# Kernel tuning notes

Hardware: AMD Instinct MI355X
Metric: run time of the kernel (lower is better)

Reference implementation:

```python
import jax, jax.numpy as jnp
import numpy as np

DIM = 1024
HEADS = 16

def setup_inputs() -> dict:
    key = jax.random.key(0)
    k1, k2, k3, k4 = jax.random.split(key, 4)
    x = jax.random.normal(k1, (2, 2048, DIM), dtype=jnp.float32)
    ln_gamma = jnp.ones((DIM,), dtype=jnp.float32)
    ln_beta = jnp.zeros((DIM,), dtype=jnp.float32)
    # torch Linear weight is [out, in]; store transposed [in, out] for x @ W
    W_qkv = jax.random.normal(k2, (DIM, 3 * DIM), dtype=jnp.float32) * (DIM ** -0.5)
    W_out = jax.random.normal(k3, (DIM, DIM), dtype=jnp.float32) * (DIM ** -0.5)
    b_out = jax.random.normal(k4, (DIM,), dtype=jnp.float32) * 0.02
    return {"x": x, "ln_gamma": ln_gamma, "ln_beta": ln_beta,
            "W_qkv": W_qkv, "W_out": W_out, "b_out": b_out}

def reference(x, ln_gamma, ln_beta, W_qkv, W_out, b_out):
    B, N, C = x.shape
    H = HEADS
    Dh = C // H
    scale = Dh ** -0.5
    # LayerNorm (eps=1e-5, torch default)
    mu = jnp.mean(x, axis=-1, keepdims=True)
    var = jnp.var(x, axis=-1, keepdims=True)
    xn = (x - mu) / jnp.sqrt(var + 1e-5) * ln_gamma + ln_beta
    # QKV projection: [B,N,3C] -> [3,B,H,N,Dh]
    qkv = (xn @ W_qkv).reshape(B, N, 3, H, Dh).transpose(2, 0, 3, 1, 4)
    q, k, v = qkv[0], qkv[1], qkv[2]
    attn = jnp.einsum('bhnd,bhmd->bhnm', q, k) * scale  # [B,H,N,N]
    attn = jax.nn.softmax(attn, axis=-1)
    out = jnp.einsum('bhnm,bhmd->bhnd', attn, v)  # [B,H,N,Dh]
    out = out.transpose(0, 2, 1, 3).reshape(B, N, C)
    return out @ W_out + b_out
```

## Files before the change

kernel.cpp:

```cpp
#include <hip/hip_runtime.h>
#include <hip/hip_bf16.h>

#define DIM 1024
#define HEADS 16
#define DH 64
#define SEQ 2048
#define BATCH 2
#define ROWS (BATCH*SEQ)
#define C3 (3*DIM)
#define NT (SEQ/64)

typedef __attribute__((ext_vector_type(8))) short s16x8;
typedef __attribute__((ext_vector_type(4))) short s16x4;
typedef __attribute__((ext_vector_type(4))) float f32x4;
typedef __attribute__((ext_vector_type(16))) float f32x16;
typedef __attribute__((ext_vector_type(4))) unsigned int u32x4;
typedef __attribute__((ext_vector_type(2))) unsigned int u32x2;

__device__ __forceinline__ void gll16(const void* g, void* l) {
  __builtin_amdgcn_global_load_lds((const __attribute__((address_space(1))) void*)g,
                                   (__attribute__((address_space(3))) void*)l, 16, 0, 0);
}
__device__ __forceinline__ float bf2f(short s) {
  return __builtin_bit_cast(float, ((unsigned)(unsigned short)s) << 16);
}
__device__ __forceinline__ short f2bf(float f) {
  return (short)__bfloat16_as_ushort(__float2bfloat16(f));
}
__device__ __forceinline__ unsigned pk2(float a, float b) {
  unsigned lo = (unsigned)__bfloat16_as_ushort(__float2bfloat16(a));
  unsigned hh = (unsigned)__bfloat16_as_ushort(__float2bfloat16(b));
  return lo | (hh << 16);
}
__device__ __forceinline__ float fexp2(float x) {
#if __has_builtin(__builtin_amdgcn_exp2f)
  return __builtin_amdgcn_exp2f(x);
#else
  float r; asm("v_exp_f32 %0, %1" : "=v"(r) : "v"(x)); return r;
#endif
}

__global__ __launch_bounds__(256) void prep_kernel(const float* __restrict__ x,
    const float* __restrict__ gamma, const float* __restrict__ beta,
    __hip_bfloat16* __restrict__ xn,
    const float* __restrict__ Wqkv, __hip_bfloat16* __restrict__ wqkv_t,
    const float* __restrict__ Wout, __hip_bfloat16* __restrict__ wout_t) {
  const int bid = blockIdx.x;
  const int t = threadIdx.x;
  if (bid < ROWS) {
    __shared__ float red[8];
    const float4* xp = (const float4*)(x + (size_t)bid * DIM);
    float4 v = xp[t];
    float s = v.x + v.y + v.z + v.w;
    float q = v.x*v.x + v.y*v.y + v.z*v.z + v.w*v.w;
    for (int off = 32; off >= 1; off >>= 1) {
      s += __shfl_xor(s, off, 64);
      q += __shfl_xor(q, off, 64);
    }
    int w = t >> 6;
    if ((t & 63) == 0) { red[w] = s; red[4 + w] = q; }
    __syncthreads();
    s = red[0] + red[1] + red[2] + red[3];
    q = red[4] + red[5] + red[6] + red[7];
    float mu = s * (1.0f / DIM);
    float var = q * (1.0f / DIM) - mu * mu;
    float rstd = rsqrtf(var + 1e-5f);
    float4 g4 = ((const float4*)gamma)[t];
    float4 b4 = ((const float4*)beta)[t];
    __hip_bfloat16* op = xn + (size_t)bid * DIM + t * 4;
    op[0] = __float2bfloat16((v.x - mu) * rstd * g4.x + b4.x);
    op[1] = __float2bfloat16((v.y - mu) * rstd * g4.y + b4.y);
    op[2] = __float2bfloat16((v.z - mu) * rstd * g4.z + b4.z);
    op[3] = __float2bfloat16((v.w - mu) * rstd * g4.w + b4.w);
  } else {
    __shared__ float tile[32][33];
    const float* in; __hip_bfloat16* out; int R, Cn, c0, r0;
    if (bid < ROWS + 3072) {
      int id = bid - ROWS;
      in = Wqkv; out = wqkv_t; R = DIM; Cn = C3;
      c0 = (id % 96) * 32; r0 = (id / 96) * 32;
    } else {
      int id = bid - ROWS - 3072;
      in = Wout; out = wout_t; R = DIM; Cn = DIM;
      c0 = (id % 32) * 32; r0 = (id / 32) * 32;
    }
    int tx = t & 31, ty = t >> 5;
#pragma unroll
    for (int i = 0; i < 4; i++)
      tile[ty + i * 8][tx] = in[(size_t)(r0 + ty + i * 8) * Cn + c0 + tx];
    __syncthreads();
#pragma unroll
    for (int i = 0; i < 4; i++)
      out[(size_t)(c0 + ty + i * 8) * R + r0 + tx] = __float2bfloat16(tile[tx][ty + i * 8]);
  }
}

__global__ __launch_bounds__(512) void gemm192(const __hip_bfloat16* __restrict__ A,
    const __hip_bfloat16* __restrict__ Bt, __hip_bfloat16* __restrict__ C,
    int M, int Nc, int K) {
  __shared__ short lds_a[2][256 * 64];
  __shared__ short lds_b[2][192 * 64];
  const int t = threadIdx.x, l = t & 63;
  const int w = t >> 6, wr = w >> 2, wc = w & 3;
  const int m0 = blockIdx.y * 256, n0 = blockIdx.x * 192;
  const short* Ab = (const short*)A;
  const short* Bb = (const short*)Bt;
  f32x4 acc[8][3] = {};
  const int srow = t >> 3;
  const int schk = (t & 7) ^ (srow & 7);
  const int NIT = K / 64;

  {
    char* la = (char*)&lds_a[0][0];
    char* lb = (char*)&lds_b[0][0];
#pragma unroll
    for (int p = 0; p < 4; p++)
      gll16(Ab + (size_t)(m0 + p * 64 + srow) * K + schk * 8, la + p * 8192 + t * 16);
#pragma unroll
    for (int p = 0; p < 3; p++)
      gll16(Bb + (size_t)(n0 + p * 64 + srow) * K + schk * 8, lb + p * 8192 + t * 16);
  }
  for (int it = 0; it < NIT; ++it) {
    const int cur = it & 1;
    __syncthreads();
    if (it + 1 < NIT) {
      const int kk = (it + 1) * 64;
      char* la = (char*)&lds_a[cur ^ 1][0];
      char* lb = (char*)&lds_b[cur ^ 1][0];
#pragma unroll
      for (int p = 0; p < 4; p++)
        gll16(Ab + (size_t)(m0 + p * 64 + srow) * K + kk + schk * 8, la + p * 8192 + t * 16);
#pragma unroll
      for (int p = 0; p < 3; p++)
        gll16(Bb + (size_t)(n0 + p * 64 + srow) * K + kk + schk * 8, lb + p * 8192 + t * 16);
      asm volatile("s_waitcnt vmcnt(7)" ::: "memory");
    } else {
      asm volatile("s_waitcnt vmcnt(0)" ::: "memory");
    }
    __syncthreads();
    const char* la = (const char*)&lds_a[cur][0];
    const char* lb = (const char*)&lds_b[cur][0];
    s16x8 af[4], bf[3];
#define GPH_READ_A(FH, S)                                                     \
    _Pragma("unroll")                                                         \
    for (int f = 0; f < 4; f++) {                                             \
      int row = wr * 128 + (FH * 4 + f) * 16 + (l & 15);                      \
      int chk = (((S) * 4 + (l >> 4)) ^ (l & 7)) * 16;                        \
      af[f] = *(const s16x8*)(la + row * 128 + chk);                          \
    }
#define GPH_READ_B(S)                                                         \
    _Pragma("unroll")                                                         \
    for (int n = 0; n < 3; n++) {                                             \
      int row = wc * 48 + n * 16 + (l & 15);                                  \
      int chk = (((S) * 4 + (l >> 4)) ^ (l & 7)) * 16;                        \
      bf[n] = *(const s16x8*)(lb + row * 128 + chk);                          \
    }
#define GPH_MFMA(FH)                                                          \
    __builtin_amdgcn_s_barrier();                                             \
    asm volatile("s_waitcnt lgkmcnt(0)" ::: "memory");                        \
    __builtin_amdgcn_sched_barrier(0);                                        \
    __builtin_amdgcn_s_setprio(1);                                            \
    _Pragma("unroll")                                                         \
    for (int f = 0; f < 4; f++)                                               \
      _Pragma("unroll")                                                       \
      for (int n = 0; n < 3; n++)                                             \
        acc[FH * 4 + f][n] =                                                  \
            __builtin_amdgcn_mfma_f32_16x16x32_bf16(af[f], bf[n],             \
                                                    acc[FH * 4 + f][n], 0, 0, 0); \
    __builtin_amdgcn_s_setprio(0);                                            \
    __builtin_amdgcn_s_barrier();

    GPH_READ_A(0, 0) GPH_READ_B(0) GPH_MFMA(0)
    GPH_READ_A(1, 0) GPH_MFMA(1)
    GPH_READ_A(0, 1) GPH_READ_B(1) GPH_MFMA(0)
    GPH_READ_A(1, 1) GPH_MFMA(1)
#undef GPH_READ_A
#undef GPH_READ_B
#undef GPH_MFMA
  }
#pragma unroll
  for (int f = 0; f < 8; f++)
#pragma unroll
    for (int n = 0; n < 3; n++) {
      int col = n0 + wc * 48 + n * 16 + (l & 15);
#pragma unroll
      for (int r = 0; r < 4; r++) {
        int row = m0 + wr * 128 + f * 16 + (l >> 4) * 4 + r;
        C[(size_t)row * Nc + col] = __float2bfloat16(acc[f][n][r]);
      }
    }
}

__global__ __launch_bounds__(256) void gemm_out(const __hip_bfloat16* __restrict__ A,
    const __hip_bfloat16* __restrict__ Bt, float* __restrict__ C,
    const float* __restrict__ bias) {
  __shared__ short lds_a[2][128 * 32];
  __shared__ short lds_b[2][64 * 32];
  const int t = threadIdx.x, l = t & 63, w = t >> 6;
  const int wr = w >> 1, wc = w & 1;
  const int m0 = blockIdx.y * 128, n0 = blockIdx.x * 64;
  const short* Ab = (const short*)A;
  const short* Bb = (const short*)Bt;
  const int K = DIM;
  f32x4 acc[4][2] = {};
  const int srow = t >> 2, scol = (t & 3) * 8;
  {
    char* la = (char*)&lds_a[0][0];
    char* lb = (char*)&lds_b[0][0];
    gll16(Ab + (size_t)(m0 + srow) * K + scol,      la + t * 16);
    gll16(Ab + (size_t)(m0 + 64 + srow) * K + scol, la + 4096 + t * 16);
    gll16(Bb + (size_t)(n0 + srow) * K + scol,      lb + t * 16);
  }
  for (int it = 0; it < K / 32; ++it) {
    const int cur = it & 1;
    __syncthreads();
    if (it + 1 < K / 32) {
      const int kk = (it + 1) * 32;
      char* la = (char*)&lds_a[cur ^ 1][0];
      char* lb = (char*)&lds_b[cur ^ 1][0];
      gll16(Ab + (size_t)(m0 + srow) * K + kk + scol,      la + t * 16);
      gll16(Ab + (size_t)(m0 + 64 + srow) * K + kk + scol, la + 4096 + t * 16);
      gll16(Bb + (size_t)(n0 + srow) * K + kk + scol,      lb + t * 16);
      asm volatile("s_waitcnt vmcnt(3)" ::: "memory");
    } else {
      asm volatile("s_waitcnt vmcnt(0)" ::: "memory");
    }
    __syncthreads();
    s16x8 af[4], bf[2];
#pragma unroll
    for (int m = 0; m < 4; m++)
      af[m] = *(const s16x8*)&lds_a[cur][(wr * 64 + m * 16 + (l & 15)) * 32 + (l >> 4) * 8];
#pragma unroll
    for (int n = 0; n < 2; n++)
      bf[n] = *(const s16x8*)&lds_b[cur][(wc * 32 + n * 16 + (l & 15)) * 32 + (l >> 4) * 8];
#pragma unroll
    for (int m = 0; m < 4; m++)
#pragma unroll
      for (int n = 0; n < 2; n++)
        acc[m][n] = __builtin_amdgcn_mfma_f32_16x16x32_bf16(af[m], bf[n], acc[m][n], 0, 0, 0);
  }
#pragma unroll
  for (int m = 0; m < 4; m++)
#pragma unroll
    for (int n = 0; n < 2; n++) {
      int col = n0 + wc * 32 + n * 16 + (l & 15);
      float bb = bias[col];
#pragma unroll
      for (int r = 0; r < 4; r++) {
        int row = m0 + wr * 64 + m * 16 + (l >> 4) * 4 + r;
        C[(size_t)row * DIM + col] = acc[m][n][r] + bb;
      }
    }
}

__global__ __launch_bounds__(512) void attn_kernel(const __hip_bfloat16* __restrict__ qkv,
    __hip_bfloat16* __restrict__ attno) {
  const int t = threadIdx.x, l = t & 63, w = t >> 6;
  const int hi = l >> 5, lq = l & 31;
  const int bid = blockIdx.x;
  const int xcd = bid & 7, j = bid >> 3;
  const int bh = xcd + 8 * (j & 3);
  const int qb = j >> 2;
  const int b = bh >> 4, h = bh & 15;
  const short* base  = (const short*)qkv + (size_t)b * SEQ * C3 + h * DH;
  const short* kbase = base + DIM;
  const short* vbase = base + 2 * DIM;
  const int qr0 = qb * 256 + w * 32;

  __shared__ short kbuf[2][2][64 * 64];
  __shared__ short vbuf[2][2][64 * 64];

  const float SCL = 0.125f * 1.44269504089f;
  s16x8 qf[4];
#pragma unroll
  for (int dk = 0; dk < 4; dk++) {
    s16x8 raw = *(const s16x8*)(base + (size_t)(qr0 + lq) * C3 + dk * 16 + hi * 8);
#pragma unroll
    for (int j2 = 0; j2 < 8; j2++) qf[dk][j2] = f2bf(bf2f(raw[j2]) * SCL);
  }

  s16x8 ones;
#pragma unroll
  for (int j2 = 0; j2 < 8; j2++) ones[j2] = (short)0x3F80;

  f32x16 o0, o1, osum, zf;
#pragma unroll
  for (int r = 0; r < 16; r++) { o0[r] = 0.f; o1[r] = 0.f; osum[r] = 0.f; zf[r] = 0.f; }
  asm volatile("" : "+v"(zf));

  const int krow = t >> 3;
  const int ksrc = (t & 7) ^ (krow & 7);
  const int vr = t & 31, vcg = t >> 5;

#define K_STAGE(DST, ROW0)                                                      \
  gll16(kbase + (size_t)((ROW0) + krow) * C3 + ksrc * 8, (char*)(DST) + t * 16);

#define V_LOAD(VA, VB, ROW0)                                                    \
  VA = __builtin_bit_cast(u32x2, *(const s16x4*)(vbase + (size_t)((ROW0) + 2 * vr) * C3 + vcg * 4)); \
  VB = __builtin_bit_cast(u32x2, *(const s16x4*)(vbase + (size_t)((ROW0) + 2 * vr + 1) * C3 + vcg * 4));

#define V_WRITE(VD, VA, VB)                                                     \
  { char* vd_ = (char*)(VD);                                                    \
    _Pragma("unroll")                                                           \
    for (int i = 0; i < 4; i++) {                                               \
      int d = vcg * 4 + i;                                                      \
      unsigned dw = __builtin_amdgcn_perm((VB)[i >> 1], (VA)[i >> 1],           \
                                          (i & 1) ? 0x07060302u : 0x05040100u); \
      *(unsigned*)(vd_ + d * 128 + (((vr >> 2) ^ (d & 7)) * 16) + (vr & 3) * 4) = dw; } }

  {
    K_STAGE(&kbuf[0][0][0], 0)
    K_STAGE(&kbuf[0][1][0], 64)
    u32x2 va0, vb0, va1, vb1;
    V_LOAD(va0, vb0, 0)
    V_LOAD(va1, vb1, 64)
    V_WRITE(&vbuf[0][0][0], va0, vb0)
    V_WRITE(&vbuf[0][1][0], va1, vb1)
  }
  __syncthreads();

#define QK_SUB(KB, S0, S1)                                                      \
  {                                                                             \
    const char* kb_ = (const char*)(KB);                                        \
    { int chk0 = (hi ^ (l & 7)) * 16;                                           \
      s16x8 kf0 = *(const s16x8*)(kb_ + (size_t)lq * 128 + chk0);               \
      s16x8 kf1 = *(const s16x8*)(kb_ + (size_t)(32 + lq) * 128 + chk0);        \
      S0 = __builtin_amdgcn_mfma_f32_32x32x16_bf16(kf0, qf[0], zf, 0, 0, 0);    \
      S1 = __builtin_amdgcn_mfma_f32_32x32x16_bf16(kf1, qf[0], zf, 0, 0, 0); }  \
    _Pragma("unroll")                                                           \
    for (int dk = 1; dk < 4; dk++) {                                            \
      int chk = ((2 * dk + hi) ^ (l & 7)) * 16;                                 \
      s16x8 kf0 = *(const s16x8*)(kb_ + (size_t)lq * 128 + chk);                \
      s16x8 kf1 = *(const s16x8*)(kb_ + (size_t)(32 + lq) * 128 + chk);         \
      S0 = __builtin_amdgcn_mfma_f32_32x32x16_bf16(kf0, qf[dk], S0, 0, 0, 0);   \
      S1 = __builtin_amdgcn_mfma_f32_32x32x16_bf16(kf1, qf[dk], S1, 0, 0, 0);   \
    }                                                                           \
  }

#define SMPV_SUB(S0, S1, VB)                                                    \
  {                                                                             \
    const char* vbp_ = (const char*)(VB);                                       \
    _Pragma("unroll")                                                           \
    for (int r = 0; r < 16; r++) { S0[r] = fexp2(S0[r]); S1[r] = fexp2(S1[r]); }\
    _Pragma("unroll")                                                           \
    for (int n = 0; n < 2; n++) {                                               \
      const f32x16& stn = n ? S1 : S0;                                          \
      _Pragma("unroll")                                                         \
      for (int ksl = 0; ksl < 2; ksl++) {                                       \
        int rb = ksl * 8;                                                       \
        int a_ = (int)pk2(stn[rb + 0], stn[rb + 1]);                            \
        int b_ = (int)pk2(stn[rb + 2], stn[rb + 3]);                            \
        int c_ = (int)pk2(stn[rb + 4], stn[rb + 5]);                            \
        int d_ = (int)pk2(stn[rb + 6], stn[rb + 7]);                            \
        asm volatile("v_permlane32_swap_b32 %0, %1" : "+v"(a_), "+v"(c_));      \
        asm volatile("v_permlane32_swap_b32 %0, %1" : "+v"(b_), "+v"(d_));      \
        u32x4 fr;                                                               \
        fr.x = (unsigned)a_;  fr.y = (unsigned)b_;                              \
        fr.z = (unsigned)c_;  fr.w = (unsigned)d_;                              \
        s16x8 pa = __builtin_bit_cast(s16x8, fr);                               \
        int ks = n * 2 + ksl;                                                   \
        int chk = ((2 * ks + hi) ^ (l & 7)) * 16;                               \
        s16x8 vf0 = *(const s16x8*)(vbp_ + (size_t)lq * 128 + chk);             \
        s16x8 vf1 = *(const s16x8*)(vbp_ + (size_t)(32 + lq) * 128 + chk);      \
        o0   = __builtin_amdgcn_mfma_f32_32x32x16_bf16(pa, vf0, o0, 0, 0, 0);   \
        o1   = __builtin_amdgcn_mfma_f32_32x32x16_bf16(pa, vf1, o1, 0, 0, 0);   \
        osum = __builtin_amdgcn_mfma_f32_32x32x16_bf16(pa, ones, osum, 0, 0, 0);\
      }                                                                         \
    }                                                                           \
  }

  for (int it = 0; it < NT / 2; ++it) {
    const int cur = it & 1;
    const bool pf = (it + 1 < NT / 2);
    u32x2 va0, vb0, va1, vb1;
    if (pf) {
      const int kv1 = (it + 1) * 128;
      K_STAGE(&kbuf[cur ^ 1][0][0], kv1)
      K_STAGE(&kbuf[cur ^ 1][1][0], kv1 + 64)
      V_LOAD(va0, vb0, kv1)
      V_LOAD(va1, vb1, kv1 + 64)
    }
    f32x16 sa0, sa1, sb0, sb1;
    QK_SUB(&kbuf[cur][0][0], sa0, sa1)
    QK_SUB(&kbuf[cur][1][0], sb0, sb1)
    SMPV_SUB(sa0, sa1, &vbuf[cur][0][0])
    SMPV_SUB(sb0, sb1, &vbuf[cur][1][0])
    if (pf) {
      V_WRITE(&vbuf[cur ^ 1][0][0], va0, vb0)
      V_WRITE(&vbuf[cur ^ 1][1][0], va1, vb1)
    }
    __syncthreads();
  }
#undef QK_SUB
#undef SMPV_SUB
#undef K_STAGE
#undef V_LOAD
#undef V_WRITE

#pragma unroll
  for (int r = 0; r < 16; r++) {
    int qr = (r & 3) + 8 * (r >> 2) + 4 * hi;
    float ir = 1.0f / osum[r];
    size_t rowoff = (size_t)(b * SEQ + qr0 + qr) * DIM + h * DH;
    attno[rowoff + lq]      = __float2bfloat16(o0[r] * ir);
    attno[rowoff + 32 + lq] = __float2bfloat16(o1[r] * ir);
  }
}

extern "C" void kernel_launch(void* const* d_in, const int* in_sizes, int n_in,
                              void* d_out, int out_size, void* d_ws, size_t ws_size,
                              hipStream_t stream) {
  const float* x     = (const float*)d_in[0];
  const float* gamma = (const float*)d_in[1];
  const float* beta  = (const float*)d_in[2];
  const float* Wqkv  = (const float*)d_in[3];
  const float* Wout  = (const float*)d_in[4];
  const float* bout  = (const float*)d_in[5];

  __hip_bfloat16* xn     = (__hip_bfloat16*)d_ws;
  __hip_bfloat16* wqkv_t = xn + (size_t)ROWS * DIM;
  __hip_bfloat16* wout_t = wqkv_t + (size_t)C3 * DIM;
  __hip_bfloat16* qkv    = wout_t + (size_t)DIM * DIM;
  __hip_bfloat16* attno  = qkv + (size_t)ROWS * C3;

  prep_kernel<<<ROWS + 3072 + 1024, 256, 0, stream>>>(x, gamma, beta, xn,
                                                      Wqkv, wqkv_t, Wout, wout_t);
  gemm192<<<dim3(C3 / 192, ROWS / 256), 512, 0, stream>>>(xn, wqkv_t, qkv, ROWS, C3, DIM);
  attn_kernel<<<8 * BATCH * HEADS, 512, 0, stream>>>(qkv, attno);
  gemm_out<<<dim3(DIM / 64, ROWS / 128), 256, 0, stream>>>(attno, wout_t, (float*)d_out, bout);
}
```

Baseline: 118.3 us.

## Enlarge output GEMM tile to 128x128x64 with swizzled LDS and MFMA priority

Reworks the output-projection GEMM to use 128x128 tiles with a K step of 64, XOR-swizzled LDS chunks, and 4x4 MFMA fragments per wave, with barriers and s_setprio around the MFMA bursts. The goal is more reuse per LDS load and fewer bank conflicts. It also wraps the attention kernel's MFMA sections in s_setprio to favour matrix-core issue. The trade-off is fewer blocks for the output GEMM (256 vs 512), more LDS per block, and more accumulator registers.

```diff
diff --git a/kernel.cpp b/kernel.cpp
--- a/kernel.cpp
+++ b/kernel.cpp
@@ -194,61 +194,85 @@
 __global__ __launch_bounds__(256) void gemm_out(const __hip_bfloat16* __restrict__ A,
     const __hip_bfloat16* __restrict__ Bt, float* __restrict__ C,
     const float* __restrict__ bias) {
-  __shared__ short lds_a[2][128 * 32];
-  __shared__ short lds_b[2][64 * 32];
-  const int t = threadIdx.x, l = t & 63, w = t >> 6;
-  const int wr = w >> 1, wc = w & 1;
-  const int m0 = blockIdx.y * 128, n0 = blockIdx.x * 64;
+  __shared__ short lds_a[2][128 * 64];
+  __shared__ short lds_b[2][128 * 64];
+  const int t = threadIdx.x, l = t & 63;
+  const int w = t >> 6, wr = w >> 1, wc = w & 1;
+  const int m0 = blockIdx.y * 128, n0 = blockIdx.x * 128;
   const short* Ab = (const short*)A;
   const short* Bb = (const short*)Bt;
   const int K = DIM;
-  f32x4 acc[4][2] = {};
-  const int srow = t >> 2, scol = (t & 3) * 8;
+  f32x4 acc[4][4] = {};
+  const int srow = t >> 3;
+  const int schk = (t & 7) ^ (srow & 7);
+  const int NIT = K / 64;
+
   {
     char* la = (char*)&lds_a[0][0];
     char* lb = (char*)&lds_b[0][0];
-    gll16(Ab + (size_t)(m0 + srow) * K + scol,      la + t * 16);
-    gll16(Ab + (size_t)(m0 + 64 + srow) * K + scol, la + 4096 + t * 16);
-    gll16(Bb + (size_t)(n0 + srow) * K + scol,      lb + t * 16);
-  }
-  for (int it = 0; it < K / 32; ++it) {
+#pragma unroll
+    for (int p = 0; p < 4; p++) {
+      gll16(Ab + (size_t)(m0 + p * 32 + srow) * K + schk * 8, la + p * 4096 + t * 16);
+      gll16(Bb + (size_t)(n0 + p * 32 + srow) * K + schk * 8, lb + p * 4096 + t * 16);
+    }
+  }
+  for (int it = 0; it < NIT; ++it) {
     const int cur = it & 1;
     __syncthreads();
-    if (it + 1 < K / 32) {
-      const int kk = (it + 1) * 32;
+    if (it + 1 < NIT) {
+      const int kk = (it + 1) * 64;
       char* la = (char*)&lds_a[cur ^ 1][0];
       char* lb = (char*)&lds_b[cur ^ 1][0];
-      gll16(Ab + (size_t)(m0 + srow) * K + kk + scol,      la + t * 16);
-      gll16(Ab + (size_t)(m0 + 64 + srow) * K + kk + scol, la + 4096 + t * 16);
-      gll16(Bb + (size_t)(n0 + srow) * K + kk + scol,      lb + t * 16);
-      asm volatile("s_waitcnt vmcnt(3)" ::: "memory");
+#pragma unroll
+      for (int p = 0; p < 4; p++) {
+        gll16(Ab + (size_t)(m0 + p * 32 + srow) * K + kk + schk * 8, la + p * 4096 + t * 16);
+        gll16(Bb + (size_t)(n0 + p * 32 + srow) * K + kk + schk * 8, lb + p * 4096 + t * 16);
+      }
+      asm volatile("s_waitcnt vmcnt(8)" ::: "memory");
     } else {
       asm volatile("s_waitcnt vmcnt(0)" ::: "memory");
     }
     __syncthreads();
-    s16x8 af[4], bf[2];
-#pragma unroll
-    for (int m = 0; m < 4; m++)
-      af[m] = *(const s16x8*)&lds_a[cur][(wr * 64 + m * 16 + (l & 15)) * 32 + (l >> 4) * 8];
-#pragma unroll
-    for (int n = 0; n < 2; n++)
-      bf[n] = *(const s16x8*)&lds_b[cur][(wc * 32 + n * 16 + (l & 15)) * 32 + (l >> 4) * 8];
-#pragma unroll
-    for (int m = 0; m < 4; m++)
-#pragma unroll
-      for (int n = 0; n < 2; n++)
-        acc[m][n] = __builtin_amdgcn_mfma_f32_16x16x32_bf16(af[m], bf[n], acc[m][n], 0, 0, 0);
-  }
-#pragma unroll
-  for (int m = 0; m < 4; m++)
-#pragma unroll
-    for (int n = 0; n < 2; n++) {
-      int col = n0 + wc * 32 + n * 16 + (l & 15);
+    const char* la = (const char*)&lds_a[cur][0];
+    const char* lb = (const char*)&lds_b[cur][0];
+#pragma unroll
+    for (int s = 0; s < 2; s++) {
+      s16x8 af[4], bf[4];
+#pragma unroll
+      for (int f = 0; f < 4; f++) {
+        int row = wr * 64 + f * 16 + (l & 15);
+        int chk = ((s * 4 + (l >> 4)) ^ (l & 7)) * 16;
+        af[f] = *(const s16x8*)(la + row * 128 + chk);
+      }
+#pragma unroll
+      for (int n = 0; n < 4; n++) {
+        int row = wc * 64 + n * 16 + (l & 15);
+        int chk = ((s * 4 + (l >> 4)) ^ (l & 7)) * 16;
+        bf[n] = *(const s16x8*)(lb + row * 128 + chk);
+      }
+      __builtin_amdgcn_s_barrier();
+      asm volatile("s_waitcnt lgkmcnt(0)" ::: "memory");
+      __builtin_amdgcn_sched_barrier(0);
+      __builtin_amdgcn_s_setprio(1);
+#pragma unroll
+      for (int f = 0; f < 4; f++)
+#pragma unroll
+        for (int n = 0; n < 4; n++)
+          acc[f][n] = __builtin_amdgcn_mfma_f32_16x16x32_bf16(af[f], bf[n], acc[f][n], 0, 0, 0);
+      __builtin_amdgcn_s_setprio(0);
+      __builtin_amdgcn_s_barrier();
+    }
+  }
+#pragma unroll
+  for (int f = 0; f < 4; f++)
+#pragma unroll
+    for (int n = 0; n < 4; n++) {
+      int col = n0 + wc * 64 + n * 16 + (l & 15);
       float bb = bias[col];
 #pragma unroll
       for (int r = 0; r < 4; r++) {
-        int row = m0 + wr * 64 + m * 16 + (l >> 4) * 4 + r;
-        C[(size_t)row * DIM + col] = acc[m][n][r] + bb;
+        int row = m0 + wr * 64 + f * 16 + (l >> 4) * 4 + r;
+        C[(size_t)row * DIM + col] = acc[f][n][r] + bb;
       }
     }
 }
@@ -322,6 +346,7 @@
 #define QK_SUB(KB, S0, S1)                                                      \
   {                                                                             \
     const char* kb_ = (const char*)(KB);                                        \
+    __builtin_amdgcn_s_setprio(1);                                              \
     { int chk0 = (hi ^ (l & 7)) * 16;                                           \
       s16x8 kf0 = *(const s16x8*)(kb_ + (size_t)lq * 128 + chk0);               \
       s16x8 kf1 = *(const s16x8*)(kb_ + (size_t)(32 + lq) * 128 + chk0);        \
@@ -335,6 +360,7 @@
       S0 = __builtin_amdgcn_mfma_f32_32x32x16_bf16(kf0, qf[dk], S0, 0, 0, 0);   \
       S1 = __builtin_amdgcn_mfma_f32_32x32x16_bf16(kf1, qf[dk], S1, 0, 0, 0);   \
     }                                                                           \
+    __builtin_amdgcn_s_setprio(0);                                              \
   }
 
 #define SMPV_SUB(S0, S1, VB)                                                    \
@@ -362,9 +388,11 @@
         int chk = ((2 * ks + hi) ^ (l & 7)) * 16;                               \
         s16x8 vf0 = *(const s16x8*)(vbp_ + (size_t)lq * 128 + chk);             \
         s16x8 vf1 = *(const s16x8*)(vbp_ + (size_t)(32 + lq) * 128 + chk);      \
+        __builtin_amdgcn_s_setprio(1);                                          \
         o0   = __builtin_amdgcn_mfma_f32_32x32x16_bf16(pa, vf0, o0, 0, 0, 0);   \
         o1   = __builtin_amdgcn_mfma_f32_32x32x16_bf16(pa, vf1, o1, 0, 0, 0);   \
         osum = __builtin_amdgcn_mfma_f32_32x32x16_bf16(pa, ones, osum, 0, 0, 0);\
+        __builtin_amdgcn_s_setprio(0);                                          \
       }                                                                         \
     }                                                                           \
   }
@@ -427,5 +455,5 @@
                                                       Wqkv, wqkv_t, Wout, wout_t);
   gemm192<<<dim3(C3 / 192, ROWS / 256), 512, 0, stream>>>(xn, wqkv_t, qkv, ROWS, C3, DIM);
   attn_kernel<<<8 * BATCH * HEADS, 512, 0, stream>>>(qkv, attno);
-  gemm_out<<<dim3(DIM / 64, ROWS / 128), 256, 0, stream>>>(attno, wout_t, (float*)d_out, bout);
-}
+  gemm_out<<<dim3(DIM / 128, ROWS / 128), 256, 0, stream>>>(attno, wout_t, (float*)d_out, bout);
+}
```

Result: slower. 134.0 us (+13.3%).
